# Performance work log

Measured on AMD Instinct MI355X. Metric: run time of the kernel, lower is better.

## Reference

```python
import jax, jax.numpy as jnp
import numpy as np

N, G, E, H, OUT, MAX_N = 131072, 256, 384, 6, 256, 1024
DH = E // H  # 64


def _make_sizes():
    # variable-length segments summing exactly to N, each in [1, MAX_N]
    rng = np.random.default_rng(0)
    raw = rng.integers(128, 896, G).astype(np.int64)
    diff = int(N - raw.sum())
    q, r = divmod(diff, G)
    sizes = raw + q
    sizes[:r] += 1
    assert sizes.sum() == N and sizes.min() >= 1 and sizes.max() <= MAX_N
    return sizes


def setup_inputs() -> dict:
    key = jax.random.key(0)
    ks = jax.random.split(key, 8)
    s = 1.0 / np.sqrt(E)
    return {
        "node_feat": jax.random.normal(ks[0], (N, E), jnp.float32),
        "sizes": jnp.asarray(_make_sizes(), jnp.int32),
        "query": jax.random.normal(ks[1], (E,), jnp.float32),
        "Wq": jax.random.normal(ks[2], (E, E), jnp.float32) * s,
        "bq": jnp.zeros((E,), jnp.float32),
        "Wk": jax.random.normal(ks[3], (E, E), jnp.float32) * s,
        "bk": jnp.zeros((E,), jnp.float32),
        "Wv": jax.random.normal(ks[4], (E, E), jnp.float32) * s,
        "bv": jnp.zeros((E,), jnp.float32),
        "Wo": jax.random.normal(ks[5], (E, E), jnp.float32) * s,
        "bo": jnp.zeros((E,), jnp.float32),
        "Wp": jax.random.normal(ks[6], (OUT, E), jnp.float32) * s,
        "bp": jnp.zeros((OUT,), jnp.float32),
    }


def reference(node_feat, sizes, query, Wq, bq, Wk, bk, Wv, bv, Wo, bo, Wp, bp):
    # segment offsets and padded gather indices
    offsets = jnp.cumsum(sizes) - sizes                      # [G]
    pos = jnp.arange(MAX_N)
    idx = jnp.clip(offsets[:, None] + pos[None, :], 0, N - 1)  # [G, MAX_N]
    mask = pos[None, :] < sizes[:, None]                     # [G, MAX_N]

    # project K/V on the flat node table (one big GEMM), then gather into padded form
    k_flat = node_feat @ Wk.T + bk                           # [N, E]
    v_flat = node_feat @ Wv.T + bv
    k = k_flat[idx].reshape(G, MAX_N, H, DH)
    v = v_flat[idx].reshape(G, MAX_N, H, DH)

    # single shared query token, pre-scaled (PyTorch MHA scales q by 1/sqrt(head_dim))
    q = ((query @ Wq.T + bq) * (1.0 / np.sqrt(DH))).reshape(H, DH)

    scores = jnp.einsum('hd,gnhd->ghn', q, k)                # [G, H, MAX_N]
    scores = jnp.where(mask[:, None, :], scores, -1e30)
    attn = jax.nn.softmax(scores, axis=-1)
    pooled = jnp.einsum('ghn,gnhd->ghd', attn, v).reshape(G, E)

    out = pooled @ Wo.T + bo                                 # MHA out_proj
    return out @ Wp.T + bp                                   # final proj  [G, OUT]
```

## Files before the change

kernel.cpp:

```cpp
#include <hip/hip_runtime.h>
#include <math.h>

#define NN 131072
#define G  256
#define E  384
#define H  6
#define DH 64
#define OUTD 256
#define MAXN 1024

#define CHK 32
#define SLOTS 32
#define PART_STRIDE 2316

#define WS_QK   0
#define WS_C    2304
#define WS_OFF  2432
#define WS_QV   2944
#define WS_WL   3328
#define WS_M    11520
#define WS_CS   11776
#define WS_PART 12288
#define WS_WVT  (WS_PART + G*SLOTS*PART_STRIDE)
#define WS_WOT  (WS_WVT + E*E)
#define WS_WPT  (WS_WOT + E*E)

__global__ __launch_bounds__(256) void k0a_scan_qv(
    const int* __restrict__ sizes, const float* __restrict__ query,
    const float* __restrict__ Wq, const float* __restrict__ bq,
    float* __restrict__ wsf) {
  const int tid = threadIdx.x;
  if (blockIdx.x == 0) {
    __shared__ int s_scan[G];
    __shared__ int s_scan2[G];
    const int sz = sizes[tid];
    s_scan[tid] = sz;
    const int nch = (sz + CHK - 1) >> 5;
    s_scan2[tid] = nch;
    __syncthreads();
    for (int d = 1; d < G; d <<= 1) {
      int t = (tid >= d) ? s_scan[tid - d] : 0;
      int t2 = (tid >= d) ? s_scan2[tid - d] : 0;
      __syncthreads();
      s_scan[tid] += t;
      s_scan2[tid] += t2;
      __syncthreads();
    }
    ((int*)(wsf + WS_OFF))[tid] = s_scan[tid] - sz;
    const int pos = s_scan2[tid] - nch;
    ((int*)(wsf + WS_CS))[tid] = pos;
    int* wl = (int*)(wsf + WS_WL);
    for (int s = 0; s < nch; s++) wl[pos + s] = (tid << 5) | s;
    if (tid == G - 1) ((int*)(wsf + WS_M))[0] = s_scan2[G - 1];
  } else {
    const int lane = tid & 63;
    const int i = (blockIdx.x - 1) * 4 + (tid >> 6);
    float a = 0.f;
#pragma unroll
    for (int j = 0; j < 6; j++)
      a += Wq[(size_t)i * E + j * 64 + lane] * query[j * 64 + lane];
#pragma unroll
    for (int mm = 1; mm < 64; mm <<= 1) a += __shfl_xor(a, mm, 64);
    if (lane == 0) wsf[WS_QV + i] = 0.125f * (a + bq[i]);
  }
}

__global__ __launch_bounds__(256) void k0b_qk(
    const float* __restrict__ Wk, const float* __restrict__ bk,
    float* __restrict__ wsf) {
  __shared__ float qv_s[64];
  __shared__ float ps[256];
  const int h = blockIdx.x / 6, ec = blockIdx.x % 6;
  const int tid = threadIdx.x;
  if (tid < 64) qv_s[tid] = wsf[WS_QV + h * 64 + tid];
  __syncthreads();
  const int el = tid & 63, dq = tid >> 6;
  float a = 0.f;
#pragma unroll 4
  for (int d = dq * 16; d < dq * 16 + 16; d++)
    a += qv_s[d] * Wk[(size_t)(h * 64 + d) * E + ec * 64 + el];
  ps[tid] = a;
  __syncthreads();
  if (tid < 64)
    wsf[WS_QK + h * E + ec * 64 + tid] =
        ps[tid] + ps[64 + tid] + ps[128 + tid] + ps[192 + tid];
  if (ec == 0 && tid < 64) {
    float p = qv_s[tid] * bk[h * 64 + tid];
#pragma unroll
    for (int mm = 1; mm < 64; mm <<= 1) p += __shfl_xor(p, mm, 64);
    if (tid == 0) wsf[WS_C + h] = p;
  }
}

__global__ __launch_bounds__(256) void k0t_transpose(
    const float* __restrict__ Wv, const float* __restrict__ Wo,
    const float* __restrict__ Wp, float* __restrict__ wsf) {
  __shared__ float s[64][65];
  const int b = blockIdx.x;
  const float* src;
  float* dst;
  int R, tr, tc;
  if (b < 36)      { src = Wv; dst = wsf + WS_WVT; R = 384; tr = b / 6;        tc = b % 6; }
  else if (b < 72) { src = Wo; dst = wsf + WS_WOT; R = 384; tr = (b - 36) / 6; tc = (b - 36) % 6; }
  else             { src = Wp; dst = wsf + WS_WPT; R = 256; tr = (b - 72) / 6; tc = (b - 72) % 6; }
  const int r0 = tr * 64, c0 = tc * 64;
#pragma unroll
  for (int k = 0; k < 16; k++) {
    int idx = k * 256 + threadIdx.x;
    int r = idx >> 6, cc = idx & 63;
    s[r][cc] = src[(size_t)(r0 + r) * E + c0 + cc];
  }
  __syncthreads();
#pragma unroll
  for (int k = 0; k < 16; k++) {
    int idx = k * 256 + threadIdx.x;
    int cc = idx >> 6, r = idx & 63;
    dst[(size_t)(c0 + cc) * R + r0 + r] = s[r][cc];
  }
}

__global__ __launch_bounds__(256) void k12_fused(
    const float* __restrict__ x, const int* __restrict__ sizes,
    float* __restrict__ wsf) {
  __shared__ float qk_l[8 * 292];
  __shared__ float c_s[8];
  __shared__ float pe2[4][CHK * 8];
  const int tid = threadIdx.x;
  for (int idx = tid; idx < 2304; idx += 256) {
    int sub = idx / 288, r3 = idx % 288;
    int h = r3 / 48, r2 = r3 % 48, j = r2 >> 2, r = r2 & 3;
    qk_l[sub * 292 + h * 48 + j * 4 + r] =
        wsf[WS_QK + h * E + (j * 8 + sub) * 4 + r];
  }
  if (tid < 8) c_s[tid] = (tid < 6) ? wsf[WS_C + tid] : 0.f;
  __syncthreads();

  const int lane = tid & 63, w = tid >> 6;
  const int gw = blockIdx.x * 4 + w;
  const int M = ((const int*)(wsf + WS_M))[0];
  if (gw >= M) return;
  const int item = ((const int*)(wsf + WS_WL))[gw];
  const int g = item >> 5, s = item & 31;
  const int Ng = sizes[g];
  const int rem = Ng - s * CHK;
  const int clen = rem < CHK ? rem : CHK;
  const int n0 = ((const int*)(wsf + WS_OFF))[g] + s * CHK;
  float* pe = pe2[w];
  float* pslot = wsf + WS_PART + (size_t)gw * PART_STRIDE;
  const int sub = lane & 7, nod = lane >> 3;
  const float4* x4 = (const float4*)x;

  {
    float acc[4][6];
#pragma unroll
    for (int o = 0; o < 4; o++)
#pragma unroll
      for (int h = 0; h < 6; h++) acc[o][h] = 0.f;
#pragma unroll 4
    for (int j = 0; j < 12; j++) {
      float4 qk4[6];
#pragma unroll
      for (int h = 0; h < 6; h++)
        qk4[h] = *(const float4*)&qk_l[sub * 292 + h * 48 + j * 4];
      float4 xv[4];
#pragma unroll
      for (int o = 0; o < 4; o++) {
        int nn = o * 8 + nod;
        nn = nn < clen ? nn : clen - 1;
        xv[o] = x4[(size_t)(n0 + nn) * 96 + j * 8 + sub];
      }
#pragma unroll
      for (int o = 0; o < 4; o++)
#pragma unroll
        for (int h = 0; h < 6; h++)
          acc[o][h] += qk4[h].x * xv[o].x + qk4[h].y * xv[o].y
                     + qk4[h].z * xv[o].z + qk4[h].w * xv[o].w;
    }
#pragma unroll
    for (int o = 0; o < 4; o++) {
#pragma unroll
      for (int h = 0; h < 6; h++) {
        acc[o][h] += __shfl_xor(acc[o][h], 1, 64);
        acc[o][h] += __shfl_xor(acc[o][h], 2, 64);
        acc[o][h] += __shfl_xor(acc[o][h], 4, 64);
      }
      float v = acc[o][0];
#pragma unroll
      for (int h = 1; h < 6; h++) v = (sub == h) ? acc[o][h] : v;
      const int nl = o * 8 + nod;
      if (sub < 6)
        pe[nl * 8 + sub] = (nl < clen) ? v + c_s[sub] : -1.0e30f;
    }
  }

  if (lane < 32) {
    const float4 sA = *(const float4*)&pe[lane * 8];
    const float2 sB = *(const float2*)&pe[lane * 8 + 4];
    float sc[6] = {sA.x, sA.y, sA.z, sA.w, sB.x, sB.y};
    float mh[6], lh[6], eh[6];
#pragma unroll
    for (int h = 0; h < 6; h++) {
      float t = sc[h];
#pragma unroll
      for (int mm = 1; mm < 32; mm <<= 1) t = fmaxf(t, __shfl_xor(t, mm, 32));
      mh[h] = t;
      eh[h] = __expf(sc[h] - t);
    }
#pragma unroll
    for (int h = 0; h < 6; h++) {
      float t = eh[h];
#pragma unroll
      for (int mm = 1; mm < 32; mm <<= 1) t += __shfl_xor(t, mm, 32);
      lh[h] = t;
    }
    *(float4*)&pe[lane * 8] = make_float4(eh[0], eh[1], eh[2], eh[3]);
    *(float2*)&pe[lane * 8 + 4] = make_float2(eh[4], eh[5]);
    if (lane < 6) {
      float vm = mh[0], vl = lh[0];
#pragma unroll
      for (int h = 1; h < 6; h++) {
        vm = (lane == h) ? mh[h] : vm;
        vl = (lane == h) ? lh[h] : vl;
      }
      pslot[2304 + lane] = vm;
      pslot[2310 + lane] = vl;
    }
  }

  {
    float accA[6][4], accB[6][4];
#pragma unroll
    for (int h = 0; h < 6; h++)
#pragma unroll
      for (int c = 0; c < 4; c++) { accA[h][c] = 0.f; accB[h][c] = 0.f; }
    const float4* xr = x4 + (size_t)n0 * 96;
    const int colB = 64 + (lane & 31);
#pragma unroll 2
    for (int n = 0; n < clen; n++) {
      const float4 xA = xr[n * 96 + lane];
      const float4 xB = xr[n * 96 + colB];
      const float4 pA = *(const float4*)&pe[n * 8];
      const float2 pB = *(const float2*)&pe[n * 8 + 4];
      const float ph[6] = {pA.x, pA.y, pA.z, pA.w, pB.x, pB.y};
#pragma unroll
      for (int h = 0; h < 6; h++) {
        accA[h][0] += ph[h] * xA.x; accA[h][1] += ph[h] * xA.y;
        accA[h][2] += ph[h] * xA.z; accA[h][3] += ph[h] * xA.w;
        accB[h][0] += ph[h] * xB.x; accB[h][1] += ph[h] * xB.y;
        accB[h][2] += ph[h] * xB.z; accB[h][3] += ph[h] * xB.w;
      }
    }
#pragma unroll
    for (int h = 0; h < 6; h++)
      *(float4*)&pslot[h * E + lane * 4] =
          make_float4(accA[h][0], accA[h][1], accA[h][2], accA[h][3]);
    if (lane < 32)
#pragma unroll
      for (int h = 0; h < 6; h++)
        *(float4*)&pslot[h * E + 256 + lane * 4] =
            make_float4(accB[h][0], accB[h][1], accB[h][2], accB[h][3]);
  }
}

__global__ __launch_bounds__(768) void k3_group(
    const float* __restrict__ wsf, const int* __restrict__ sizes,
    const float* __restrict__ bv, const float* __restrict__ bo,
    const float* __restrict__ bp, float* __restrict__ out) {
  __shared__ float xb[H * E];
  __shared__ float pooled[E];
  __shared__ float om[E];
  __shared__ float ps[768];
  __shared__ float msh[SLOTS][H], lsh[SLOTS][H], wgt[SLOTS][H];
  __shared__ float linv[H];
  const int tid = threadIdx.x;
  const int g = blockIdx.x;
  const int nch = (sizes[g] + CHK - 1) >> 5;
  const int base_s = ((const int*)(wsf + WS_CS))[g];
  const float* pg = wsf + WS_PART + (size_t)base_s * PART_STRIDE;
  const float* wvt = wsf + WS_WVT;
  const float* wot = wsf + WS_WOT;
  const float* wpt = wsf + WS_WPT;

  if (tid < SLOTS * H) {
    const int s2 = tid / H, h2 = tid % H;
    if (s2 < nch) {
      msh[s2][h2] = pg[(size_t)s2 * PART_STRIDE + 2304 + h2];
      lsh[s2][h2] = pg[(size_t)s2 * PART_STRIDE + 2310 + h2];
    }
  }
  __syncthreads();
  if (tid < H) {
    float m = -3.0e38f;
    for (int s = 0; s < nch; s++) m = fmaxf(m, msh[s][tid]);
    float L = 0.f;
    for (int s = 0; s < nch; s++) {
      float wv_ = __expf(msh[s][tid] - m);
      wgt[s][tid] = wv_;
      L += lsh[s][tid] * wv_;
    }
    linv[tid] = 1.f / L;
  }
  __syncthreads();
  for (int idx = tid; idx < H * E; idx += 768) {
    int h = idx / E;
    float a = 0.f;
    for (int s = 0; s < nch; s++) a += pg[(size_t)s * PART_STRIDE + idx] * wgt[s][h];
    xb[idx] = a * linv[h];
  }
  __syncthreads();

  {
    const int i = tid % 384, ks = tid / 384;
    const float* xh = xb + (i >> 6) * E + ks * 192;
    const float* wp_ = wvt + (size_t)(ks * 192) * E + i;
    float a0 = 0.f, a1 = 0.f, a2 = 0.f, a3 = 0.f;
#pragma unroll 4
    for (int e = 0; e < 192; e += 4) {
      a0 += wp_[(size_t)(e + 0) * E] * xh[e + 0];
      a1 += wp_[(size_t)(e + 1) * E] * xh[e + 1];
      a2 += wp_[(size_t)(e + 2) * E] * xh[e + 2];
      a3 += wp_[(size_t)(e + 3) * E] * xh[e + 3];
    }
    ps[tid] = (a0 + a1) + (a2 + a3);
  }
  __syncthreads();
  if (tid < 384) pooled[tid] = ps[tid] + ps[384 + tid] + bv[tid];
  __syncthreads();

  {
    const int i = tid % 384, ks = tid / 384;
    const float* xh = pooled + ks * 192;
    const float* wp_ = wot + (size_t)(ks * 192) * E + i;
    float a0 = 0.f, a1 = 0.f, a2 = 0.f, a3 = 0.f;
#pragma unroll 4
    for (int e = 0; e < 192; e += 4) {
      a0 += wp_[(size_t)(e + 0) * E] * xh[e + 0];
      a1 += wp_[(size_t)(e + 1) * E] * xh[e + 1];
      a2 += wp_[(size_t)(e + 2) * E] * xh[e + 2];
      a3 += wp_[(size_t)(e + 3) * E] * xh[e + 3];
    }
    ps[tid] = (a0 + a1) + (a2 + a3);
  }
  __syncthreads();
  if (tid < 384) om[tid] = ps[tid] + ps[384 + tid] + bo[tid];
  __syncthreads();

  {
    const int o = tid % 256, ks = tid / 256;
    const float* xh = om + ks * 128;
    const float* wp_ = wpt + (size_t)(ks * 128) * OUTD + o;
    float a0 = 0.f, a1 = 0.f, a2 = 0.f, a3 = 0.f;
#pragma unroll 4
    for (int e = 0; e < 128; e += 4) {
      a0 += wp_[(size_t)(e + 0) * OUTD] * xh[e + 0];
      a1 += wp_[(size_t)(e + 1) * OUTD] * xh[e + 1];
      a2 += wp_[(size_t)(e + 2) * OUTD] * xh[e + 2];
      a3 += wp_[(size_t)(e + 3) * OUTD] * xh[e + 3];
    }
    ps[tid] = (a0 + a1) + (a2 + a3);
  }
  __syncthreads();
  if (tid < 256)
    out[(size_t)g * OUTD + tid] = ps[tid] + ps[256 + tid] + ps[512 + tid] + bp[tid];
}

extern "C" void kernel_launch(void* const* d_in, const int* in_sizes, int n_in,
                              void* d_out, int out_size, void* d_ws, size_t ws_size,
                              hipStream_t stream) {
  const float* x     = (const float*)d_in[0];
  const int*   sizes = (const int*)d_in[1];
  const float* query = (const float*)d_in[2];
  const float* Wq    = (const float*)d_in[3];
  const float* bq    = (const float*)d_in[4];
  const float* Wk    = (const float*)d_in[5];
  const float* bk    = (const float*)d_in[6];
  const float* Wv    = (const float*)d_in[7];
  const float* bv    = (const float*)d_in[8];
  const float* Wo    = (const float*)d_in[9];
  const float* bo    = (const float*)d_in[10];
  const float* Wp    = (const float*)d_in[11];
  const float* bp    = (const float*)d_in[12];
  float* wsf = (float*)d_ws;
  float* out = (float*)d_out;

  hipLaunchKernelGGL(k0a_scan_qv, dim3(97), dim3(256), 0, stream,
                     sizes, query, Wq, bq, wsf);
  hipLaunchKernelGGL(k0b_qk, dim3(36), dim3(256), 0, stream, Wk, bk, wsf);
  hipLaunchKernelGGL(k0t_transpose, dim3(96), dim3(256), 0, stream,
                     Wv, Wo, Wp, wsf);
  hipLaunchKernelGGL(k12_fused, dim3(1088), dim3(256), 0, stream,
                     x, sizes, wsf);
  hipLaunchKernelGGL(k3_group, dim3(G), dim3(768), 0, stream,
                     wsf, sizes, bv, bo, bp, out);
}
```

Measured before the change: 375.2 us.

## Split each chunk work item across two wavefronts in k12_fused

Each 32-node chunk is now handled by a 128-thread block of two waves instead of a single wave, so there is one block per work item and the grid grows to 4352. Score computation is divided by node halves, and the weighted V accumulation is divided by columns: wave 0 takes columns 0-255 and wave 1 takes columns 256-383, with two node parities reduced by a shuffle. This removes the idle half-wave in the old column-B pass and doubles parallelism per item. The cost is extra block barriers, reloading the qk table into shared memory for every block, and an uneven split of columns between the two waves.

```diff
diff --git a/kernel.cpp b/kernel.cpp
--- a/kernel.cpp
+++ b/kernel.cpp
@@ -119,41 +119,40 @@
   }
 }
 
-__global__ __launch_bounds__(256) void k12_fused(
+__global__ __launch_bounds__(128, 6) void k12_fused(
     const float* __restrict__ x, const int* __restrict__ sizes,
     float* __restrict__ wsf) {
   __shared__ float qk_l[8 * 292];
   __shared__ float c_s[8];
-  __shared__ float pe2[4][CHK * 8];
-  const int tid = threadIdx.x;
-  for (int idx = tid; idx < 2304; idx += 256) {
-    int sub = idx / 288, r3 = idx % 288;
-    int h = r3 / 48, r2 = r3 % 48, j = r2 >> 2, r = r2 & 3;
-    qk_l[sub * 292 + h * 48 + j * 4 + r] =
-        wsf[WS_QK + h * E + (j * 8 + sub) * 4 + r];
-  }
-  if (tid < 8) c_s[tid] = (tid < 6) ? wsf[WS_C + tid] : 0.f;
-  __syncthreads();
-
-  const int lane = tid & 63, w = tid >> 6;
-  const int gw = blockIdx.x * 4 + w;
+  __shared__ float pe[CHK * 8];
   const int M = ((const int*)(wsf + WS_M))[0];
-  if (gw >= M) return;
-  const int item = ((const int*)(wsf + WS_WL))[gw];
+  if ((int)blockIdx.x >= M) return;
+  const int item = ((const int*)(wsf + WS_WL))[blockIdx.x];
   const int g = item >> 5, s = item & 31;
   const int Ng = sizes[g];
   const int rem = Ng - s * CHK;
   const int clen = rem < CHK ? rem : CHK;
   const int n0 = ((const int*)(wsf + WS_OFF))[g] + s * CHK;
-  float* pe = pe2[w];
-  float* pslot = wsf + WS_PART + (size_t)gw * PART_STRIDE;
+  const int tid = threadIdx.x;
+  const int lane = tid & 63, w = tid >> 6;
+
+  for (int idx = tid; idx < 2304; idx += 128) {
+    int sub = idx / 288, r3 = idx % 288;
+    int h = r3 / 48, r2 = r3 % 48, j = r2 >> 2, r = r2 & 3;
+    qk_l[sub * 292 + h * 48 + j * 4 + r] =
+        wsf[WS_QK + h * E + (j * 8 + sub) * 4 + r];
+  }
+  if (tid < 8) c_s[tid] = (tid < 6) ? wsf[WS_C + tid] : 0.f;
+  __syncthreads();
+
   const int sub = lane & 7, nod = lane >> 3;
   const float4* x4 = (const float4*)x;
+  float* pslot = wsf + WS_PART + (size_t)blockIdx.x * PART_STRIDE;
 
   {
-    float acc[4][6];
-#pragma unroll
-    for (int o = 0; o < 4; o++)
+    float acc[2][6];
+#pragma unroll
+    for (int o = 0; o < 2; o++)
 #pragma unroll
       for (int h = 0; h < 6; h++) acc[o][h] = 0.f;
 #pragma unroll 4
@@ -162,22 +161,22 @@
 #pragma unroll
       for (int h = 0; h < 6; h++)
         qk4[h] = *(const float4*)&qk_l[sub * 292 + h * 48 + j * 4];
-      float4 xv[4];
-#pragma unroll
-      for (int o = 0; o < 4; o++) {
-        int nn = o * 8 + nod;
+      float4 xv[2];
+#pragma unroll
+      for (int o = 0; o < 2; o++) {
+        int nn = w * 16 + o * 8 + nod;
         nn = nn < clen ? nn : clen - 1;
         xv[o] = x4[(size_t)(n0 + nn) * 96 + j * 8 + sub];
       }
 #pragma unroll
-      for (int o = 0; o < 4; o++)
+      for (int o = 0; o < 2; o++)
 #pragma unroll
         for (int h = 0; h < 6; h++)
           acc[o][h] += qk4[h].x * xv[o].x + qk4[h].y * xv[o].y
                      + qk4[h].z * xv[o].z + qk4[h].w * xv[o].w;
     }
 #pragma unroll
-    for (int o = 0; o < 4; o++) {
+    for (int o = 0; o < 2; o++) {
 #pragma unroll
       for (int h = 0; h < 6; h++) {
         acc[o][h] += __shfl_xor(acc[o][h], 1, 64);
@@ -187,13 +186,14 @@
       float v = acc[o][0];
 #pragma unroll
       for (int h = 1; h < 6; h++) v = (sub == h) ? acc[o][h] : v;
-      const int nl = o * 8 + nod;
+      const int nl = w * 16 + o * 8 + nod;
       if (sub < 6)
         pe[nl * 8 + sub] = (nl < clen) ? v + c_s[sub] : -1.0e30f;
     }
   }
-
-  if (lane < 32) {
+  __syncthreads();
+
+  if (w == 0 && lane < 32) {
     const float4 sA = *(const float4*)&pe[lane * 8];
     const float2 sB = *(const float2*)&pe[lane * 8 + 4];
     float sc[6] = {sA.x, sA.y, sA.z, sA.w, sB.x, sB.y};
@@ -226,39 +226,63 @@
       pslot[2310 + lane] = vl;
     }
   }
-
-  {
-    float accA[6][4], accB[6][4];
+  __syncthreads();
+
+  const float4* xr = x4 + (size_t)n0 * 96;
+  if (w == 0) {
+    float acc[6][4];
 #pragma unroll
     for (int h = 0; h < 6; h++)
 #pragma unroll
-      for (int c = 0; c < 4; c++) { accA[h][c] = 0.f; accB[h][c] = 0.f; }
-    const float4* xr = x4 + (size_t)n0 * 96;
-    const int colB = 64 + (lane & 31);
+      for (int c = 0; c < 4; c++) acc[h][c] = 0.f;
 #pragma unroll 2
     for (int n = 0; n < clen; n++) {
       const float4 xA = xr[n * 96 + lane];
-      const float4 xB = xr[n * 96 + colB];
       const float4 pA = *(const float4*)&pe[n * 8];
       const float2 pB = *(const float2*)&pe[n * 8 + 4];
       const float ph[6] = {pA.x, pA.y, pA.z, pA.w, pB.x, pB.y};
 #pragma unroll
       for (int h = 0; h < 6; h++) {
-        accA[h][0] += ph[h] * xA.x; accA[h][1] += ph[h] * xA.y;
-        accA[h][2] += ph[h] * xA.z; accA[h][3] += ph[h] * xA.w;
-        accB[h][0] += ph[h] * xB.x; accB[h][1] += ph[h] * xB.y;
-        accB[h][2] += ph[h] * xB.z; accB[h][3] += ph[h] * xB.w;
+        acc[h][0] += ph[h] * xA.x; acc[h][1] += ph[h] * xA.y;
+        acc[h][2] += ph[h] * xA.z; acc[h][3] += ph[h] * xA.w;
       }
     }
 #pragma unroll
     for (int h = 0; h < 6; h++)
       *(float4*)&pslot[h * E + lane * 4] =
-          make_float4(accA[h][0], accA[h][1], accA[h][2], accA[h][3]);
+          make_float4(acc[h][0], acc[h][1], acc[h][2], acc[h][3]);
+  } else {
+    float acc[6][4];
+#pragma unroll
+    for (int h = 0; h < 6; h++)
+#pragma unroll
+      for (int c = 0; c < 4; c++) acc[h][c] = 0.f;
+    const int colB = 64 + (lane & 31);
+    const int par = lane >> 5;
+#pragma unroll 2
+    for (int n = 0; n < CHK; n += 2) {
+      const int nl = n + par;
+      int nn = nl < clen ? nl : clen - 1;
+      const float4 xB = xr[nn * 96 + colB];
+      const float4 pA = *(const float4*)&pe[nl * 8];
+      const float2 pB = *(const float2*)&pe[nl * 8 + 4];
+      const float ph[6] = {pA.x, pA.y, pA.z, pA.w, pB.x, pB.y};
+#pragma unroll
+      for (int h = 0; h < 6; h++) {
+        acc[h][0] += ph[h] * xB.x; acc[h][1] += ph[h] * xB.y;
+        acc[h][2] += ph[h] * xB.z; acc[h][3] += ph[h] * xB.w;
+      }
+    }
+#pragma unroll
+    for (int h = 0; h < 6; h++)
+#pragma unroll
+      for (int c = 0; c < 4; c++)
+        acc[h][c] += __shfl_xor(acc[h][c], 32, 64);
     if (lane < 32)
 #pragma unroll
       for (int h = 0; h < 6; h++)
         *(float4*)&pslot[h * E + 256 + lane * 4] =
-            make_float4(accB[h][0], accB[h][1], accB[h][2], accB[h][3]);
+            make_float4(acc[h][0], acc[h][1], acc[h][2], acc[h][3]);
   }
 }
 
@@ -388,7 +412,7 @@
   hipLaunchKernelGGL(k0b_qk, dim3(36), dim3(256), 0, stream, Wk, bk, wsf);
   hipLaunchKernelGGL(k0t_transpose, dim3(96), dim3(256), 0, stream,
                      Wv, Wo, Wp, wsf);
-  hipLaunchKernelGGL(k12_fused, dim3(1088), dim3(256), 0, stream,
+  hipLaunchKernelGGL(k12_fused, dim3(4352), dim3(128), 0, stream,
                      x, sizes, wsf);
   hipLaunchKernelGGL(k3_group, dim3(G), dim3(768), 0, stream,
                      wsf, sizes, bv, bo, bp, out);
```

After: 366.7 us. 1.02x faster.
